# Optimization experiments

Hardware: AMD Instinct MI355X
Metric: run time of the kernel (lower is better)

The kernel has to match this reference:

```python
import jax, jax.numpy as jnp
import numpy as np

H = 1024   # hidden_size
L = 4      # num_layers
S = 5      # parallel LSTM streams (l, r, f2l, f2r, h2h)
IN = 42    # 21 keypoints * 2 coords per stream
A = 256    # attention_dim
C = 500    # num_classes


def _params(key):
    ks = jax.random.split(key, 13)
    sc = 1.0 / np.sqrt(H)
    n = jax.random.normal
    return dict(
        W_ih0=n(ks[0], (S, 4 * H, IN)) * sc,        # layer-0 input weights
        W_ihr=n(ks[1], (S, L - 1, 4 * H, H)) * sc,  # layers 1.. input weights
        W_hh=n(ks[2], (S, L, 4 * H, H)) * sc,
        b_ih=n(ks[3], (S, L, 4 * H)) * sc,
        b_hh=n(ks[4], (S, L, 4 * H)) * sc,
        fuse_w=n(ks[5], (H, S * H)) * sc,
        fuse_b=n(ks[6], (H,)) * sc,
        att_w=n(ks[7], (A, H)) * sc,
        att_b=n(ks[8], (A,)) * sc,
        score_w=n(ks[9], (1, A)) * sc,
        score_b=n(ks[10], (1,)) * sc,
        fc_w=n(ks[11], (C, H)) * sc,
        fc_b=n(ks[12], (C,)) * sc,
    )


def setup_inputs():
    key = jax.random.key(0)
    kx, kp = jax.random.split(key)
    inp = {"x": jax.random.normal(kx, (1, 133, 2), dtype=jnp.float32)}
    inp.update(_params(kp))
    return inp


def _prepare(x):
    # x: [1, 133, 2] whole-body keypoints -> [5, 42] per-stream feature vectors
    p = x[0].astype(jnp.float32)
    src_body, src_left, src_right = p[0], p[100], p[121]
    body, left, right = p[:17], p[91:112], p[112:133]
    w_l = left[:, 0].max() - left[:, 0].min()
    h_l = left[:, 1].max() - left[:, 1].min()
    w_r = right[:, 0].max() - right[:, 0].min()
    h_r = right[:, 1].max() - right[:, 1].min()
    w_b = body[5, 0] - body[6, 0]
    h_b = 4.0 * w_b
    f2l = left - src_body
    f2r = right - src_body
    h2h = left - right
    left = left - src_left
    right = right - src_right
    one = jnp.float32(1.0)
    cl = (w_l != 0) & (h_l != 0)
    left = left / jnp.stack([jnp.where(cl, w_l, one), jnp.where(cl, h_l, one)])
    cr = (w_r != 0) & (h_r != 0)
    right = right / jnp.stack([jnp.where(cr, w_r, one), jnp.where(cr, h_r, one)])
    cb = (w_b != 0) & (h_b != 0)
    wb = jnp.where(cb, w_b, one)
    hb = jnp.where(cb, h_b, one)
    f2l = f2l / jnp.stack([wb, one])   # only x scaled (matches torch)
    f2r = f2r / jnp.stack([one, hb])   # only y scaled (matches torch)
    h2h = h2h / jnp.stack([wb, hb])
    return jnp.concatenate([left, right, f2l, f2r, h2h]).reshape(S, IN)


def reference(x, W_ih0, W_ihr, W_hh, b_ih, b_hh, fuse_w, fuse_b,
              att_w, att_b, score_w, score_b, fc_w, fc_b):
    xs = _prepare(x)                                   # [S, IN]
    h0 = jnp.zeros((S, H), jnp.float32)                # zero initial states
    c0 = jnp.zeros((S, H), jnp.float32)
    inp = xs
    for layer in range(L):                             # stacked single-step LSTM
        Wih = W_ih0 if layer == 0 else W_ihr[:, layer - 1]
        gates = (jnp.einsum('sgi,si->sg', Wih, inp)
                 + jnp.einsum('sgh,sh->sg', W_hh[:, layer], h0)
                 + b_ih[:, layer] + b_hh[:, layer])    # [S, 4H]; order i,f,g,o
        i, f, g, o = jnp.split(gates, 4, axis=-1)
        c = jax.nn.sigmoid(f) * c0 + jax.nn.sigmoid(i) * jnp.tanh(g)
        inp = jax.nn.sigmoid(o) * jnp.tanh(c)          # becomes next layer input
    fused = inp.reshape(1, S * H) @ fuse_w.T + fuse_b  # [1, H]
    lstm_out = fused[:, None, :]                       # [1, 1, H]
    aw = jnp.tanh(lstm_out @ att_w.T + att_b)          # [1, 1, A]
    scores = jax.nn.softmax(aw @ score_w.T + score_b, axis=1)  # [1,1,1]
    ctx = jnp.sum(scores * lstm_out, axis=1)           # [1, H]
    return ctx @ fc_w.T + fc_b                         # [1, C]
```

## Files before the change

kernel.cpp:

```cpp
#include <hip/hip_runtime.h>
#include <math.h>

#define HH   1024
#define SS   5
#define LL   4
#define INW  42
#define CC   500

#define WS_XS     0
#define WS_HA     256
#define WS_HB     5632
#define WS_FUSED  11008

__device__ __forceinline__ float sigf(float v) { return 1.0f / (1.0f + expf(-v)); }

__device__ __forceinline__ float wave_sum(float v) {
#pragma unroll
    for (int m = 32; m >= 1; m >>= 1) v += __shfl_xor(v, m, 64);
    return v;
}

__global__ void prep_kernel(const float* __restrict__ x, float* __restrict__ xs) {
    int t = threadIdx.x;
    const float sbx = x[0 * 2 + 0],   sby = x[0 * 2 + 1];
    const float slx = x[100 * 2 + 0], sly = x[100 * 2 + 1];
    const float srx = x[121 * 2 + 0], sry = x[121 * 2 + 1];

    float lminx = 1e30f, lmaxx = -1e30f, lminy = 1e30f, lmaxy = -1e30f;
    float rminx = 1e30f, rmaxx = -1e30f, rminy = 1e30f, rmaxy = -1e30f;
    for (int i = 0; i < 21; ++i) {
        float lx = x[(91 + i) * 2 + 0], ly = x[(91 + i) * 2 + 1];
        float rx = x[(112 + i) * 2 + 0], ry = x[(112 + i) * 2 + 1];
        lminx = fminf(lminx, lx); lmaxx = fmaxf(lmaxx, lx);
        lminy = fminf(lminy, ly); lmaxy = fmaxf(lmaxy, ly);
        rminx = fminf(rminx, rx); rmaxx = fmaxf(rmaxx, rx);
        rminy = fminf(rminy, ry); rmaxy = fmaxf(rmaxy, ry);
    }
    float w_l = lmaxx - lminx, h_l = lmaxy - lminy;
    float w_r = rmaxx - rminx, h_r = rmaxy - rminy;
    float w_b = x[5 * 2 + 0] - x[6 * 2 + 0];
    float h_b = 4.0f * w_b;

    bool cl = (w_l != 0.0f) && (h_l != 0.0f);
    float dlx = cl ? w_l : 1.0f, dly = cl ? h_l : 1.0f;
    bool cr = (w_r != 0.0f) && (h_r != 0.0f);
    float drx = cr ? w_r : 1.0f, dry = cr ? h_r : 1.0f;
    bool cb = (w_b != 0.0f) && (h_b != 0.0f);
    float wb = cb ? w_b : 1.0f, hb = cb ? h_b : 1.0f;

    if (t < 105) {
        int grp = t / 21, i = t % 21;
        float lx = x[(91 + i) * 2 + 0], ly = x[(91 + i) * 2 + 1];
        float rx = x[(112 + i) * 2 + 0], ry = x[(112 + i) * 2 + 1];
        float ox = 0.0f, oy = 0.0f;
        switch (grp) {
            case 0: ox = (lx - slx) / dlx; oy = (ly - sly) / dly; break;
            case 1: ox = (rx - srx) / drx; oy = (ry - sry) / dry; break;
            case 2: ox = (lx - sbx) / wb;  oy = (ly - sby);       break;
            case 3: ox = (rx - sbx);       oy = (ry - sby) / hb;  break;
            case 4: ox = (lx - rx) / wb;   oy = (ly - ry) / hb;   break;
        }
        xs[t * 2 + 0] = ox;
        xs[t * 2 + 1] = oy;
    }
}

__global__ __launch_bounds__(256) void layer0_kernel(
    const float* __restrict__ W,
    const float* __restrict__ b_ih,
    const float* __restrict__ b_hh,
    const float* __restrict__ xs,
    float* __restrict__ hout)
{
    int wid = (blockIdx.x << 2) + (threadIdx.x >> 6);
    int lane = threadIdx.x & 63;
    int s = wid >> 10, j = wid & 1023;

    const float* Ws = W + (size_t)s * 4096 * INW;
    float ai = 0.0f, ag = 0.0f, ao = 0.0f;
    if (lane < INW) {
        float xv = xs[s * INW + lane];
        ai = Ws[(size_t)(j) * INW + lane] * xv;
        ag = Ws[(size_t)(2048 + j) * INW + lane] * xv;
        ao = Ws[(size_t)(3072 + j) * INW + lane] * xv;
    }
    ai = wave_sum(ai); ag = wave_sum(ag); ao = wave_sum(ao);

    if (lane == 0) {
        const float* bi = b_ih + (size_t)(s * LL + 0) * 4096;
        const float* bh = b_hh + (size_t)(s * LL + 0) * 4096;
        float gi = ai + bi[j] + bh[j];
        float gg = ag + bi[2048 + j] + bh[2048 + j];
        float go = ao + bi[3072 + j] + bh[3072 + j];
        float c = sigf(gi) * tanhf(gg);
        hout[s * HH + j] = sigf(go) * tanhf(c);
    }
}

__global__ __launch_bounds__(256) void layer_kernel(
    const float* __restrict__ W,
    const float* __restrict__ b_ih,
    const float* __restrict__ b_hh,
    int layer,
    const float* __restrict__ hin,
    float* __restrict__ hout)
{
    int wid = (blockIdx.x << 2) + (threadIdx.x >> 6);
    int lane = threadIdx.x & 63;
    int s = wid >> 10, j = wid & 1023;

    const float* Ws = W + (size_t)(s * (LL - 1) + (layer - 1)) * 4096 * HH;
    const float4* ri = (const float4*)(Ws + (size_t)(j) * HH);
    const float4* rg = (const float4*)(Ws + (size_t)(2048 + j) * HH);
    const float4* ro = (const float4*)(Ws + (size_t)(3072 + j) * HH);
    const float4* hv = (const float4*)(hin + s * HH);

    float ai = 0.0f, ag = 0.0f, ao = 0.0f;
#pragma unroll
    for (int k = 0; k < 4; ++k) {
        int idx = (k << 6) + lane;
        float4 h4 = hv[idx];
        float4 wi = ri[idx];
        float4 wg = rg[idx];
        float4 wo = ro[idx];
        ai += wi.x * h4.x + wi.y * h4.y + wi.z * h4.z + wi.w * h4.w;
        ag += wg.x * h4.x + wg.y * h4.y + wg.z * h4.z + wg.w * h4.w;
        ao += wo.x * h4.x + wo.y * h4.y + wo.z * h4.z + wo.w * h4.w;
    }
    ai = wave_sum(ai); ag = wave_sum(ag); ao = wave_sum(ao);

    if (lane == 0) {
        const float* bi = b_ih + (size_t)(s * LL + layer) * 4096;
        const float* bh = b_hh + (size_t)(s * LL + layer) * 4096;
        float gi = ai + bi[j] + bh[j];
        float gg = ag + bi[2048 + j] + bh[2048 + j];
        float go = ao + bi[3072 + j] + bh[3072 + j];
        float c = sigf(gi) * tanhf(gg);
        hout[s * HH + j] = sigf(go) * tanhf(c);
    }
}

__global__ __launch_bounds__(256) void fuse_kernel(
    const float* __restrict__ fw,
    const float* __restrict__ fb,
    const float* __restrict__ hflat,
    float* __restrict__ fused)
{
    int wid = (blockIdx.x << 2) + (threadIdx.x >> 6);
    int lane = threadIdx.x & 63;
    int j = wid;

    const float4* row = (const float4*)(fw + (size_t)j * (SS * HH));
    const float4* hv = (const float4*)hflat;
    float a = 0.0f;
#pragma unroll
    for (int k = 0; k < 20; ++k) {
        int idx = (k << 6) + lane;
        float4 w = row[idx];
        float4 h = hv[idx];
        a += w.x * h.x + w.y * h.y + w.z * h.z + w.w * h.w;
    }
    a = wave_sum(a);
    if (lane == 0) fused[j] = a + fb[j];
}

__global__ __launch_bounds__(256) void fc_kernel(
    const float* __restrict__ fw,
    const float* __restrict__ fb,
    const float* __restrict__ fused,
    float* __restrict__ out)
{
    int wid = (blockIdx.x << 2) + (threadIdx.x >> 6);
    int lane = threadIdx.x & 63;
    int c = wid;
    if (c >= CC) return;

    const float4* row = (const float4*)(fw + (size_t)c * HH);
    const float4* hv = (const float4*)fused;
    float a = 0.0f;
#pragma unroll
    for (int k = 0; k < 4; ++k) {
        int idx = (k << 6) + lane;
        float4 w = row[idx];
        float4 h = hv[idx];
        a += w.x * h.x + w.y * h.y + w.z * h.z + w.w * h.w;
    }
    a = wave_sum(a);
    if (lane == 0) out[c] = a + fb[c];
}

extern "C" void kernel_launch(void* const* d_in, const int* in_sizes, int n_in,
                              void* d_out, int out_size, void* d_ws, size_t ws_size,
                              hipStream_t stream) {
    const float* x      = (const float*)d_in[0];
    const float* W_ih0  = (const float*)d_in[1];
    const float* W_ihr  = (const float*)d_in[2];
    const float* b_ih   = (const float*)d_in[4];
    const float* b_hh   = (const float*)d_in[5];
    const float* fuse_w = (const float*)d_in[6];
    const float* fuse_b = (const float*)d_in[7];
    const float* fc_w   = (const float*)d_in[12];
    const float* fc_b   = (const float*)d_in[13];
    float* out = (float*)d_out;

    float* ws    = (float*)d_ws;
    float* xs    = ws + WS_XS;
    float* hA    = ws + WS_HA;
    float* hB    = ws + WS_HB;
    float* fused = ws + WS_FUSED;

    prep_kernel<<<1, 128, 0, stream>>>(x, xs);
    layer0_kernel<<<1280, 256, 0, stream>>>(W_ih0, b_ih, b_hh, xs, hA);
    layer_kernel<<<1280, 256, 0, stream>>>(W_ihr, b_ih, b_hh, 1, hA, hB);
    layer_kernel<<<1280, 256, 0, stream>>>(W_ihr, b_ih, b_hh, 2, hB, hA);
    layer_kernel<<<1280, 256, 0, stream>>>(W_ihr, b_ih, b_hh, 3, hA, hB);
    fuse_kernel<<<256, 256, 0, stream>>>(fuse_w, fuse_b, hB, fused);
    fc_kernel<<<125, 256, 0, stream>>>(fc_w, fc_b, fused, out);
}
```

Before: 548.8 us.

## Fuse all stages into one cooperative kernel with grid syncs

Replaces the seven separate launches (prep, four LSTM layers, fuse, fc) with one cooperative kernel of 640 blocks that uses grid.sync between stages. Each wave now computes two hidden units, so it issues six row loads per step to add memory-level parallelism. The aim is to remove launch overhead and inter-kernel gaps. In exchange it relies on every block being co-resident and pays the cost of grid-wide barriers, and each wave recomputes the cheap input preparation.

```diff
diff --git a/kernel.cpp b/kernel.cpp
--- a/kernel.cpp
+++ b/kernel.cpp
@@ -1,5 +1,8 @@
 #include <hip/hip_runtime.h>
+#include <hip/hip_cooperative_groups.h>
 #include <math.h>
+
+namespace cg = cooperative_groups;
 
 #define HH   1024
 #define SS   5
@@ -7,11 +10,6 @@
 #define INW  42
 #define CC   500
 
-#define WS_XS     0
-#define WS_HA     256
-#define WS_HB     5632
-#define WS_FUSED  11008
-
 __device__ __forceinline__ float sigf(float v) { return 1.0f / (1.0f + expf(-v)); }
 
 __device__ __forceinline__ float wave_sum(float v) {
@@ -20,173 +18,176 @@
     return v;
 }
 
-__global__ void prep_kernel(const float* __restrict__ x, float* __restrict__ xs) {
-    int t = threadIdx.x;
-    const float sbx = x[0 * 2 + 0],   sby = x[0 * 2 + 1];
-    const float slx = x[100 * 2 + 0], sly = x[100 * 2 + 1];
-    const float srx = x[121 * 2 + 0], sry = x[121 * 2 + 1];
-
-    float lminx = 1e30f, lmaxx = -1e30f, lminy = 1e30f, lmaxy = -1e30f;
-    float rminx = 1e30f, rmaxx = -1e30f, rminy = 1e30f, rmaxy = -1e30f;
-    for (int i = 0; i < 21; ++i) {
-        float lx = x[(91 + i) * 2 + 0], ly = x[(91 + i) * 2 + 1];
-        float rx = x[(112 + i) * 2 + 0], ry = x[(112 + i) * 2 + 1];
-        lminx = fminf(lminx, lx); lmaxx = fmaxf(lmaxx, lx);
-        lminy = fminf(lminy, ly); lmaxy = fmaxf(lmaxy, ly);
-        rminx = fminf(rminx, rx); rmaxx = fmaxf(rmaxx, rx);
-        rminy = fminf(rminy, ry); rmaxy = fmaxf(rmaxy, ry);
-    }
-    float w_l = lmaxx - lminx, h_l = lmaxy - lminy;
-    float w_r = rmaxx - rminx, h_r = rmaxy - rminy;
-    float w_b = x[5 * 2 + 0] - x[6 * 2 + 0];
-    float h_b = 4.0f * w_b;
-
-    bool cl = (w_l != 0.0f) && (h_l != 0.0f);
-    float dlx = cl ? w_l : 1.0f, dly = cl ? h_l : 1.0f;
-    bool cr = (w_r != 0.0f) && (h_r != 0.0f);
-    float drx = cr ? w_r : 1.0f, dry = cr ? h_r : 1.0f;
-    bool cb = (w_b != 0.0f) && (h_b != 0.0f);
-    float wb = cb ? w_b : 1.0f, hb = cb ? h_b : 1.0f;
-
-    if (t < 105) {
-        int grp = t / 21, i = t % 21;
-        float lx = x[(91 + i) * 2 + 0], ly = x[(91 + i) * 2 + 1];
-        float rx = x[(112 + i) * 2 + 0], ry = x[(112 + i) * 2 + 1];
-        float ox = 0.0f, oy = 0.0f;
-        switch (grp) {
-            case 0: ox = (lx - slx) / dlx; oy = (ly - sly) / dly; break;
-            case 1: ox = (rx - srx) / drx; oy = (ry - sry) / dry; break;
-            case 2: ox = (lx - sbx) / wb;  oy = (ly - sby);       break;
-            case 3: ox = (rx - sbx);       oy = (ry - sby) / hb;  break;
-            case 4: ox = (lx - rx) / wb;   oy = (ly - ry) / hb;   break;
-        }
-        xs[t * 2 + 0] = ox;
-        xs[t * 2 + 1] = oy;
-    }
-}
-
-__global__ __launch_bounds__(256) void layer0_kernel(
-    const float* __restrict__ W,
+__global__ __launch_bounds__(256, 3) void fused_all(
+    const float* __restrict__ x,
+    const float* __restrict__ W_ih0,
+    const float* __restrict__ W_ihr,
     const float* __restrict__ b_ih,
     const float* __restrict__ b_hh,
-    const float* __restrict__ xs,
-    float* __restrict__ hout)
+    const float* __restrict__ fuse_w,
+    const float* __restrict__ fuse_b,
+    const float* __restrict__ fc_w,
+    const float* __restrict__ fc_b,
+    float* __restrict__ out,
+    float* __restrict__ ws)
 {
-    int wid = (blockIdx.x << 2) + (threadIdx.x >> 6);
-    int lane = threadIdx.x & 63;
-    int s = wid >> 10, j = wid & 1023;
-
-    const float* Ws = W + (size_t)s * 4096 * INW;
-    float ai = 0.0f, ag = 0.0f, ao = 0.0f;
-    if (lane < INW) {
-        float xv = xs[s * INW + lane];
-        ai = Ws[(size_t)(j) * INW + lane] * xv;
-        ag = Ws[(size_t)(2048 + j) * INW + lane] * xv;
-        ao = Ws[(size_t)(3072 + j) * INW + lane] * xv;
-    }
-    ai = wave_sum(ai); ag = wave_sum(ag); ao = wave_sum(ao);
-
-    if (lane == 0) {
-        const float* bi = b_ih + (size_t)(s * LL + 0) * 4096;
-        const float* bh = b_hh + (size_t)(s * LL + 0) * 4096;
-        float gi = ai + bi[j] + bh[j];
-        float gg = ag + bi[2048 + j] + bh[2048 + j];
-        float go = ao + bi[3072 + j] + bh[3072 + j];
-        float c = sigf(gi) * tanhf(gg);
-        hout[s * HH + j] = sigf(go) * tanhf(c);
-    }
-}
-
-__global__ __launch_bounds__(256) void layer_kernel(
-    const float* __restrict__ W,
-    const float* __restrict__ b_ih,
-    const float* __restrict__ b_hh,
-    int layer,
-    const float* __restrict__ hin,
-    float* __restrict__ hout)
-{
-    int wid = (blockIdx.x << 2) + (threadIdx.x >> 6);
-    int lane = threadIdx.x & 63;
-    int s = wid >> 10, j = wid & 1023;
-
-    const float* Ws = W + (size_t)(s * (LL - 1) + (layer - 1)) * 4096 * HH;
-    const float4* ri = (const float4*)(Ws + (size_t)(j) * HH);
-    const float4* rg = (const float4*)(Ws + (size_t)(2048 + j) * HH);
-    const float4* ro = (const float4*)(Ws + (size_t)(3072 + j) * HH);
-    const float4* hv = (const float4*)(hin + s * HH);
-
-    float ai = 0.0f, ag = 0.0f, ao = 0.0f;
-#pragma unroll
-    for (int k = 0; k < 4; ++k) {
-        int idx = (k << 6) + lane;
-        float4 h4 = hv[idx];
-        float4 wi = ri[idx];
-        float4 wg = rg[idx];
-        float4 wo = ro[idx];
-        ai += wi.x * h4.x + wi.y * h4.y + wi.z * h4.z + wi.w * h4.w;
-        ag += wg.x * h4.x + wg.y * h4.y + wg.z * h4.z + wg.w * h4.w;
-        ao += wo.x * h4.x + wo.y * h4.y + wo.z * h4.z + wo.w * h4.w;
-    }
-    ai = wave_sum(ai); ag = wave_sum(ag); ao = wave_sum(ao);
-
-    if (lane == 0) {
-        const float* bi = b_ih + (size_t)(s * LL + layer) * 4096;
-        const float* bh = b_hh + (size_t)(s * LL + layer) * 4096;
-        float gi = ai + bi[j] + bh[j];
-        float gg = ag + bi[2048 + j] + bh[2048 + j];
-        float go = ao + bi[3072 + j] + bh[3072 + j];
-        float c = sigf(gi) * tanhf(gg);
-        hout[s * HH + j] = sigf(go) * tanhf(c);
-    }
-}
-
-__global__ __launch_bounds__(256) void fuse_kernel(
-    const float* __restrict__ fw,
-    const float* __restrict__ fb,
-    const float* __restrict__ hflat,
-    float* __restrict__ fused)
-{
-    int wid = (blockIdx.x << 2) + (threadIdx.x >> 6);
-    int lane = threadIdx.x & 63;
-    int j = wid;
-
-    const float4* row = (const float4*)(fw + (size_t)j * (SS * HH));
-    const float4* hv = (const float4*)hflat;
-    float a = 0.0f;
-#pragma unroll
-    for (int k = 0; k < 20; ++k) {
-        int idx = (k << 6) + lane;
-        float4 w = row[idx];
-        float4 h = hv[idx];
-        a += w.x * h.x + w.y * h.y + w.z * h.z + w.w * h.w;
-    }
-    a = wave_sum(a);
-    if (lane == 0) fused[j] = a + fb[j];
-}
-
-__global__ __launch_bounds__(256) void fc_kernel(
-    const float* __restrict__ fw,
-    const float* __restrict__ fb,
-    const float* __restrict__ fused,
-    float* __restrict__ out)
-{
-    int wid = (blockIdx.x << 2) + (threadIdx.x >> 6);
-    int lane = threadIdx.x & 63;
-    int c = wid;
-    if (c >= CC) return;
-
-    const float4* row = (const float4*)(fw + (size_t)c * HH);
-    const float4* hv = (const float4*)fused;
-    float a = 0.0f;
-#pragma unroll
-    for (int k = 0; k < 4; ++k) {
-        int idx = (k << 6) + lane;
-        float4 w = row[idx];
-        float4 h = hv[idx];
-        a += w.x * h.x + w.y * h.y + w.z * h.z + w.w * h.w;
-    }
-    a = wave_sum(a);
-    if (lane == 0) out[c] = a + fb[c];
+    cg::grid_group grid = cg::this_grid();
+    const int wid  = (blockIdx.x << 2) + (threadIdx.x >> 6);
+    const int lane = threadIdx.x & 63;
+    const int s    = wid >> 9;
+    const int j0   = (wid & 511) << 1;
+
+    float* hA    = ws;
+    float* hB    = ws + 5120;
+    float* fused = ws + 10240;
+
+    {
+        const float sbx = x[0],   sby = x[1];
+        const float slx = x[200], sly = x[201];
+        const float srx = x[242], sry = x[243];
+        float lminx = 1e30f, lmaxx = -1e30f, lminy = 1e30f, lmaxy = -1e30f;
+        float rminx = 1e30f, rmaxx = -1e30f, rminy = 1e30f, rmaxy = -1e30f;
+        for (int i = 0; i < 21; ++i) {
+            float lx = x[(91 + i) * 2 + 0], ly = x[(91 + i) * 2 + 1];
+            float rx = x[(112 + i) * 2 + 0], ry = x[(112 + i) * 2 + 1];
+            lminx = fminf(lminx, lx); lmaxx = fmaxf(lmaxx, lx);
+            lminy = fminf(lminy, ly); lmaxy = fmaxf(lmaxy, ly);
+            rminx = fminf(rminx, rx); rmaxx = fmaxf(rmaxx, rx);
+            rminy = fminf(rminy, ry); rmaxy = fmaxf(rmaxy, ry);
+        }
+        float w_l = lmaxx - lminx, h_l = lmaxy - lminy;
+        float w_r = rmaxx - rminx, h_r = rmaxy - rminy;
+        float w_b = x[10] - x[12];
+        float h_b = 4.0f * w_b;
+        bool cl = (w_l != 0.0f) && (h_l != 0.0f);
+        float dlx = cl ? w_l : 1.0f, dly = cl ? h_l : 1.0f;
+        bool cr = (w_r != 0.0f) && (h_r != 0.0f);
+        float drx = cr ? w_r : 1.0f, dry = cr ? h_r : 1.0f;
+        bool cb = (w_b != 0.0f) && (h_b != 0.0f);
+        float wb = cb ? w_b : 1.0f, hb = cb ? h_b : 1.0f;
+
+        float xv = 0.0f;
+        if (lane < INW) {
+            int idx = s * INW + lane;
+            int p = idx >> 1, coord = idx & 1;
+            int grp = p / 21, i = p % 21;
+            float lc = x[(91 + i) * 2 + coord];
+            float rc = x[(112 + i) * 2 + coord];
+            switch (grp) {
+                case 0: xv = (lc - (coord ? sly : slx)) / (coord ? dly : dlx); break;
+                case 1: xv = (rc - (coord ? sry : srx)) / (coord ? dry : drx); break;
+                case 2: xv = (lc - (coord ? sby : sbx)) / (coord ? 1.0f : wb); break;
+                case 3: xv = (rc - (coord ? sby : sbx)) / (coord ? hb : 1.0f); break;
+                default: xv = (lc - rc) / (coord ? hb : wb); break;
+            }
+        }
+
+        const float* Ws = W_ih0 + (size_t)s * 4096 * INW;
+        float a0 = 0, a1 = 0, a2 = 0, a3 = 0, a4 = 0, a5 = 0;
+        if (lane < INW) {
+            a0 = Ws[(size_t)(j0) * INW + lane] * xv;
+            a1 = Ws[(size_t)(j0 + 1) * INW + lane] * xv;
+            a2 = Ws[(size_t)(2048 + j0) * INW + lane] * xv;
+            a3 = Ws[(size_t)(2048 + j0 + 1) * INW + lane] * xv;
+            a4 = Ws[(size_t)(3072 + j0) * INW + lane] * xv;
+            a5 = Ws[(size_t)(3072 + j0 + 1) * INW + lane] * xv;
+        }
+        a0 = wave_sum(a0); a1 = wave_sum(a1); a2 = wave_sum(a2);
+        a3 = wave_sum(a3); a4 = wave_sum(a4); a5 = wave_sum(a5);
+
+        if (lane == 0) {
+            const float* bi = b_ih + (size_t)(s * LL + 0) * 4096;
+            const float* bh = b_hh + (size_t)(s * LL + 0) * 4096;
+            float gi0 = a0 + bi[j0] + bh[j0];
+            float gi1 = a1 + bi[j0 + 1] + bh[j0 + 1];
+            float gg0 = a2 + bi[2048 + j0] + bh[2048 + j0];
+            float gg1 = a3 + bi[2048 + j0 + 1] + bh[2048 + j0 + 1];
+            float go0 = a4 + bi[3072 + j0] + bh[3072 + j0];
+            float go1 = a5 + bi[3072 + j0 + 1] + bh[3072 + j0 + 1];
+            hA[s * HH + j0]     = sigf(go0) * tanhf(sigf(gi0) * tanhf(gg0));
+            hA[s * HH + j0 + 1] = sigf(go1) * tanhf(sigf(gi1) * tanhf(gg1));
+        }
+    }
+    __threadfence();
+    grid.sync();
+
+#pragma unroll
+    for (int layer = 1; layer < LL; ++layer) {
+        const float* hin  = (layer & 1) ? hA : hB;
+        float*       hout = (layer & 1) ? hB : hA;
+
+        const float* Ws = W_ihr + (size_t)(s * (LL - 1) + (layer - 1)) * 4096 * HH;
+        const float4* r0 = (const float4*)(Ws + (size_t)(j0) * HH);
+        const float4* r1 = (const float4*)(Ws + (size_t)(j0 + 1) * HH);
+        const float4* r2 = (const float4*)(Ws + (size_t)(2048 + j0) * HH);
+        const float4* r3 = (const float4*)(Ws + (size_t)(2048 + j0 + 1) * HH);
+        const float4* r4 = (const float4*)(Ws + (size_t)(3072 + j0) * HH);
+        const float4* r5 = (const float4*)(Ws + (size_t)(3072 + j0 + 1) * HH);
+        const float4* hv = (const float4*)(hin + s * HH);
+
+        float a0 = 0, a1 = 0, a2 = 0, a3 = 0, a4 = 0, a5 = 0;
+#pragma unroll
+        for (int k = 0; k < 4; ++k) {
+            int idx = (k << 6) + lane;
+            float4 h4 = hv[idx];
+            float4 w;
+            w = r0[idx]; a0 += w.x * h4.x + w.y * h4.y + w.z * h4.z + w.w * h4.w;
+            w = r1[idx]; a1 += w.x * h4.x + w.y * h4.y + w.z * h4.z + w.w * h4.w;
+            w = r2[idx]; a2 += w.x * h4.x + w.y * h4.y + w.z * h4.z + w.w * h4.w;
+            w = r3[idx]; a3 += w.x * h4.x + w.y * h4.y + w.z * h4.z + w.w * h4.w;
+            w = r4[idx]; a4 += w.x * h4.x + w.y * h4.y + w.z * h4.z + w.w * h4.w;
+            w = r5[idx]; a5 += w.x * h4.x + w.y * h4.y + w.z * h4.z + w.w * h4.w;
+        }
+        a0 = wave_sum(a0); a1 = wave_sum(a1); a2 = wave_sum(a2);
+        a3 = wave_sum(a3); a4 = wave_sum(a4); a5 = wave_sum(a5);
+
+        if (lane == 0) {
+            const float* bi = b_ih + (size_t)(s * LL + layer) * 4096;
+            const float* bh = b_hh + (size_t)(s * LL + layer) * 4096;
+            float gi0 = a0 + bi[j0] + bh[j0];
+            float gi1 = a1 + bi[j0 + 1] + bh[j0 + 1];
+            float gg0 = a2 + bi[2048 + j0] + bh[2048 + j0];
+            float gg1 = a3 + bi[2048 + j0 + 1] + bh[2048 + j0 + 1];
+            float go0 = a4 + bi[3072 + j0] + bh[3072 + j0];
+            float go1 = a5 + bi[3072 + j0 + 1] + bh[3072 + j0 + 1];
+            hout[s * HH + j0]     = sigf(go0) * tanhf(sigf(gi0) * tanhf(gg0));
+            hout[s * HH + j0 + 1] = sigf(go1) * tanhf(sigf(gi1) * tanhf(gg1));
+        }
+        __threadfence();
+        grid.sync();
+    }
+
+    if (wid < HH) {
+        const float4* row = (const float4*)(fuse_w + (size_t)wid * (SS * HH));
+        const float4* hv  = (const float4*)hB;
+        float a = 0.0f;
+#pragma unroll
+        for (int k = 0; k < 20; ++k) {
+            int idx = (k << 6) + lane;
+            float4 w = row[idx];
+            float4 h = hv[idx];
+            a += w.x * h.x + w.y * h.y + w.z * h.z + w.w * h.w;
+        }
+        a = wave_sum(a);
+        if (lane == 0) fused[wid] = a + fuse_b[wid];
+    }
+    __threadfence();
+    grid.sync();
+
+    if (wid < CC) {
+        const float4* row = (const float4*)(fc_w + (size_t)wid * HH);
+        const float4* hv  = (const float4*)fused;
+        float a = 0.0f;
+#pragma unroll
+        for (int k = 0; k < 4; ++k) {
+            int idx = (k << 6) + lane;
+            float4 w = row[idx];
+            float4 h = hv[idx];
+            a += w.x * h.x + w.y * h.y + w.z * h.z + w.w * h.w;
+        }
+        a = wave_sum(a);
+        if (lane == 0) out[wid] = a + fc_b[wid];
+    }
 }
 
 extern "C" void kernel_launch(void* const* d_in, const int* in_sizes, int n_in,
@@ -202,18 +203,11 @@
     const float* fc_w   = (const float*)d_in[12];
     const float* fc_b   = (const float*)d_in[13];
     float* out = (float*)d_out;
-
-    float* ws    = (float*)d_ws;
-    float* xs    = ws + WS_XS;
-    float* hA    = ws + WS_HA;
-    float* hB    = ws + WS_HB;
-    float* fused = ws + WS_FUSED;
-
-    prep_kernel<<<1, 128, 0, stream>>>(x, xs);
-    layer0_kernel<<<1280, 256, 0, stream>>>(W_ih0, b_ih, b_hh, xs, hA);
-    layer_kernel<<<1280, 256, 0, stream>>>(W_ihr, b_ih, b_hh, 1, hA, hB);
-    layer_kernel<<<1280, 256, 0, stream>>>(W_ihr, b_ih, b_hh, 2, hB, hA);
-    layer_kernel<<<1280, 256, 0, stream>>>(W_ihr, b_ih, b_hh, 3, hA, hB);
-    fuse_kernel<<<256, 256, 0, stream>>>(fuse_w, fuse_b, hB, fused);
-    fc_kernel<<<125, 256, 0, stream>>>(fc_w, fc_b, fused, out);
+    float* wsf = (float*)d_ws;
+
+    void* args[] = { (void*)&x, (void*)&W_ih0, (void*)&W_ihr, (void*)&b_ih,
+                     (void*)&b_hh, (void*)&fuse_w, (void*)&fuse_b, (void*)&fc_w,
+                     (void*)&fc_b, (void*)&out, (void*)&wsf };
+    hipLaunchCooperativeKernel((const void*)fused_all, dim3(640), dim3(256),
+                               args, 0, stream);
 }
```

Result: slower. 1.170 ms (+113.1%).
